# Optimization experiments

Measured on AMD Instinct MI355X. Metric: run time of the kernel, lower is better.

## Reference

```python
import jax, jax.numpy as jnp
import numpy as np

B, T, C = 8, 2048, 1024
E = 8            # num_experts (= world_size in the original)
K = 2            # top-k
CAP_FACTOR = 1.25
CAPACITY = int(T / E * CAP_FACTOR)  # 320, per (expert, batch-row)
DFF = 4 * C


def setup_inputs() -> dict:
    key = jax.random.key(0)
    ks = jax.random.split(key, 4)
    x = jax.random.normal(ks[0], (B, T, C), dtype=jnp.float32)
    Wg = jax.random.normal(ks[1], (C, E), dtype=jnp.float32) * (C ** -0.5)
    bg = jnp.zeros((E,), dtype=jnp.float32)
    W1 = jax.random.normal(ks[2], (E, C, DFF), dtype=jnp.float32) * (C ** -0.5)
    b1 = jnp.zeros((E, DFF), dtype=jnp.float32)
    W2 = jax.random.normal(ks[3], (E, DFF, C), dtype=jnp.float32) * (DFF ** -0.5)
    b2 = jnp.zeros((E, C), dtype=jnp.float32)
    return {"x": x, "Wg": Wg, "bg": bg, "W1": W1, "b1": b1, "W2": W2, "b2": b2}


def reference(x, Wg, bg, W1, b1, W2, b2):
    # Router: linear + softmax, then top-k gating
    probs = jax.nn.softmax(jnp.einsum('btc,ce->bte', x, Wg) + bg, axis=-1)  # [B,T,E]
    topk_p, topk_e = jax.lax.top_k(probs, K)                               # [B,T,K]

    S = T * K  # one "assignment" per (token, k-slot), row-major (t, k) order
    e_flat = topk_e.reshape(B, S)                      # expert id per assignment
    p_flat = topk_p.reshape(B, S)

    # Position of each assignment within its (batch-row, expert) group,
    # ordered by token position then k-slot (matches nonzero() row-major order).
    onehot = (e_flat[..., None] == jnp.arange(E)).astype(jnp.int32)        # [B,S,E]
    pos_all = jnp.cumsum(onehot, axis=1) - 1                                # [B,S,E]
    pos = jnp.take_along_axis(pos_all, e_flat[..., None], axis=2)[..., 0]   # [B,S]
    keep = pos < CAPACITY                               # overflow tokens are dropped

    # Dispatch tokens into padded per-(expert,row) buffers: [E,B,CAPACITY,C]
    x_rep = jnp.repeat(x, K, axis=1)                    # [B,S,C], assignment order
    b_idx = jnp.broadcast_to(jnp.arange(B)[:, None], (B, S))
    pos_scat = jnp.where(keep, pos, CAPACITY)           # out-of-range -> dropped
    dispatch = jnp.zeros((E, B, CAPACITY, C), dtype=x.dtype)
    dispatch = dispatch.at[e_flat, b_idx, pos_scat].set(x_rep, mode='drop')

    # Grouped expert FFN (padding rows are zeros; their outputs are never read back)
    h = jax.nn.relu(jnp.einsum('ebsc,ech->ebsh', dispatch, W1) + b1[:, None, None, :])
    y = jnp.einsum('ebsh,ehc->ebsc', h, W2) + b2[:, None, None, :]

    # Combine: gather back, scale by gate prob (dropped tokens -> padding_val 0)
    gathered = y[e_flat, b_idx, jnp.clip(pos, 0, CAPACITY - 1)]             # [B,S,C]
    out = gathered * jnp.where(keep, p_flat, 0.0)[..., None]
    return out.reshape(B, T, K, C).sum(axis=2)          # sum over k assignments
```

## Files before the change

### kernel.cpp

```cpp
#include <hip/hip_runtime.h>
#include <stdint.h>

#define B_ 8
#define T_ 2048
#define C_ 1024
#define E_ 8
#define K_ 2
#define CAP_ 320
#define DFF_ 4096
#define S_ (T_*K_)
#define NTOK (B_*T_)
#define ROWS_PER_E (B_*CAP_)

typedef __attribute__((ext_vector_type(8))) short short8;
typedef __attribute__((ext_vector_type(4))) float floatx4;

__device__ __forceinline__ unsigned short f2bf(float f) {
  union { float f; unsigned u; } v; v.f = f;
  unsigned r = v.u + 0x7fffu + ((v.u >> 16) & 1u);
  return (unsigned short)(r >> 16);
}
__device__ __forceinline__ float bf2f(unsigned short h) {
  union { unsigned u; float f; } v; v.u = ((unsigned)h) << 16;
  return v.f;
}

__global__ void router_kernel(const float* __restrict__ x, const float* __restrict__ Wg,
                              const float* __restrict__ bg,
                              int* __restrict__ topk_e, float* __restrict__ topk_p)
{
  int token = (int)((blockIdx.x * blockDim.x + threadIdx.x) >> 6);
  int lane = threadIdx.x & 63;
  if (token >= NTOK) return;
  const float* xr = x + (size_t)token * C_;
  double acc[E_];
  #pragma unroll
  for (int e = 0; e < E_; ++e) acc[e] = 0.0;
  for (int c = lane; c < C_; c += 64) {
    double xv = (double)xr[c];
    const float4* w4 = (const float4*)(Wg + (size_t)c * E_);
    float4 wa = w4[0], wb = w4[1];
    acc[0] += xv * (double)wa.x; acc[1] += xv * (double)wa.y;
    acc[2] += xv * (double)wa.z; acc[3] += xv * (double)wa.w;
    acc[4] += xv * (double)wb.x; acc[5] += xv * (double)wb.y;
    acc[6] += xv * (double)wb.z; acc[7] += xv * (double)wb.w;
  }
  #pragma unroll
  for (int off = 32; off; off >>= 1) {
    #pragma unroll
    for (int e = 0; e < E_; ++e) acc[e] += __shfl_down(acc[e], off, 64);
  }
  if (lane == 0) {
    double lg[E_];
    double mx = -1e300;
    #pragma unroll
    for (int e = 0; e < E_; ++e) { lg[e] = acc[e] + (double)bg[e]; mx = fmax(mx, lg[e]); }
    double se = 0.0, pr[E_];
    #pragma unroll
    for (int e = 0; e < E_; ++e) { pr[e] = exp(lg[e] - mx); se += pr[e]; }
    #pragma unroll
    for (int e = 0; e < E_; ++e) pr[e] /= se;
    int e0 = 0;
    #pragma unroll
    for (int e = 1; e < E_; ++e) if (pr[e] > pr[e0]) e0 = e;
    int e1 = -1;
    #pragma unroll
    for (int e = 0; e < E_; ++e) {
      if (e == e0) continue;
      if (e1 < 0 || pr[e] > pr[e1]) e1 = e;
    }
    topk_e[token*2+0] = e0; topk_p[token*2+0] = (float)pr[e0];
    topk_e[token*2+1] = e1; topk_p[token*2+1] = (float)pr[e1];
  }
}

__global__ void scan_kernel(const int* __restrict__ topk_e,
                            int* __restrict__ pos_arr,
                            int* __restrict__ slot_src,
                            int* __restrict__ counts)
{
  const int b = blockIdx.x;
  const int tid = threadIdx.x;
  const int PT = S_ / 256;
  __shared__ int cnt[256][E_];
  int e_loc[16];
  int local[E_];
  #pragma unroll
  for (int e = 0; e < E_; ++e) local[e] = 0;
  const int* te = topk_e + (size_t)b * S_;
  for (int j = 0; j < PT; ++j) {
    int e = te[tid*PT + j];
    e_loc[j] = e;
    local[e]++;
  }
  #pragma unroll
  for (int e = 0; e < E_; ++e) cnt[tid][e] = local[e];
  __syncthreads();
  if (tid < E_) {
    int run = 0;
    for (int i = 0; i < 256; ++i) { int v = cnt[i][tid]; cnt[i][tid] = run; run += v; }
    counts[tid*B_ + b] = run;
  }
  __syncthreads();
  int base[E_];
  #pragma unroll
  for (int e = 0; e < E_; ++e) base[e] = cnt[tid][e];
  for (int j = 0; j < PT; ++j) {
    int e = e_loc[j];
    int p = base[e]++;
    int s = tid*PT + j;
    if (p < CAP_) {
      pos_arr[(size_t)b*S_ + s] = p;
      slot_src[((size_t)e*B_ + b)*CAP_ + p] = s >> 1;
    } else {
      pos_arr[(size_t)b*S_ + s] = -1;
    }
  }
}

__global__ void transpose_conv_kernel(const float* __restrict__ in, unsigned short* __restrict__ out,
                                      int R, int Cc)
{
  __shared__ float tile[32][33];
  const int e = blockIdx.z;
  const float* ine = in + (size_t)e * R * Cc;
  unsigned short* oute = out + (size_t)e * R * Cc;
  const int c0 = blockIdx.x * 32, r0 = blockIdx.y * 32;
  const int tx = threadIdx.x & 7, ty = threadIdx.x >> 3;
  float4 v = *(const float4*)(ine + (size_t)(r0 + ty) * Cc + c0 + tx*4);
  tile[ty][tx*4+0] = v.x; tile[ty][tx*4+1] = v.y;
  tile[ty][tx*4+2] = v.z; tile[ty][tx*4+3] = v.w;
  __syncthreads();
  ushort4 o;
  o.x = f2bf(tile[tx*4+0][ty]);
  o.y = f2bf(tile[tx*4+1][ty]);
  o.z = f2bf(tile[tx*4+2][ty]);
  o.w = f2bf(tile[tx*4+3][ty]);
  *(ushort4*)(oute + (size_t)(c0 + ty) * R + r0 + tx*4) = o;
}

__global__ void dispatch_kernel(const float* __restrict__ x, const int* __restrict__ slot_src,
                                const int* __restrict__ counts, unsigned short* __restrict__ Xd,
                                int e_base, int nexp)
{
  int row = (int)((blockIdx.x * blockDim.x + threadIdx.x) >> 6);
  int lane = threadIdx.x & 63;
  int total = nexp * B_ * CAP_;
  if (row >= total) return;
  int el = row / (B_*CAP_);
  int rem = row - el*(B_*CAP_);
  int b = rem / CAP_, slot = rem - b*CAP_;
  int eg = e_base + el;
  int cnt = counts[eg*B_ + b]; if (cnt > CAP_) cnt = CAP_;
  unsigned short* orow = Xd + (size_t)row * C_;
  if (slot < cnt) {
    int t = slot_src[((size_t)eg*B_ + b)*CAP_ + slot];
    const float4* xr = (const float4*)(x + ((size_t)b*T_ + t)*C_);
    #pragma unroll
    for (int i = 0; i < C_/256; ++i) {
      float4 v = xr[i*64 + lane];
      ushort4 o;
      o.x = f2bf(v.x); o.y = f2bf(v.y); o.z = f2bf(v.z); o.w = f2bf(v.w);
      ((ushort4*)orow)[i*64 + lane] = o;
    }
  } else {
    ushort4 z; z.x = z.y = z.z = z.w = 0;
    #pragma unroll
    for (int i = 0; i < C_/256; ++i) ((ushort4*)orow)[i*64 + lane] = z;
  }
}

template<int RELU>
__global__ __launch_bounds__(256, 2) void gemm_bt_kernel(
    const unsigned short* __restrict__ A,
    const unsigned short* __restrict__ BT,
    const float* __restrict__ bias,
    unsigned short* __restrict__ Out,
    int M, int N, int K)
{
  __shared__ __align__(16) unsigned short ldsA[128*32];
  __shared__ __align__(16) unsigned short ldsB[128*32];
  const int e = blockIdx.z;
  const unsigned short* Ae = A + (size_t)e * M * K;
  const unsigned short* Be = BT + (size_t)e * N * K;
  const float* be = bias + (size_t)e * N;
  unsigned short* Oe = Out + (size_t)e * M * N;
  const int m0 = blockIdx.y * 128, n0 = blockIdx.x * 128;
  const int tid = threadIdx.x, lane = tid & 63, w = tid >> 6;
  const int wr = w >> 1, wc = w & 1;

  floatx4 acc[4][4];
  #pragma unroll
  for (int i = 0; i < 4; ++i)
    #pragma unroll
    for (int j = 0; j < 4; ++j) acc[i][j] = (floatx4){0.f, 0.f, 0.f, 0.f};

  const int c0 = tid, c1 = tid + 256;
  const int ar0 = c0 >> 2, ap0 = (c0 & 3) * 8;
  const int ar1 = c1 >> 2, ap1 = (c1 & 3) * 8;
  const unsigned short* agp0 = Ae + (size_t)(m0 + ar0)*K + ap0;
  const unsigned short* agp1 = Ae + (size_t)(m0 + ar1)*K + ap1;
  const unsigned short* bgp0 = Be + (size_t)(n0 + ar0)*K + ap0;
  const unsigned short* bgp1 = Be + (size_t)(n0 + ar1)*K + ap1;

  short8 sA0 = *(const short8*)(agp0);
  short8 sA1 = *(const short8*)(agp1);
  short8 sB0 = *(const short8*)(bgp0);
  short8 sB1 = *(const short8*)(bgp1);

  short8* wAp = (short8*)ldsA;
  short8* wBp = (short8*)ldsB;

  const int fRow = lane & 15, fK = (lane >> 4) * 8;
  const unsigned short* raBase = ldsA + (size_t)(wr*64 + fRow)*32 + fK;
  const unsigned short* rbBase = ldsB + (size_t)(wc*64 + fRow)*32 + fK;

  const int nk = K / 32;
  for (int kt = 0; kt < nk; ++kt) {
    __syncthreads();
    wAp[c0] = sA0; wAp[c1] = sA1;
    wBp[c0] = sB0; wBp[c1] = sB1;
    __syncthreads();
    if (kt + 1 < nk) {
      const int koff = (kt + 1) * 32;
      sA0 = *(const short8*)(agp0 + koff);
      sA1 = *(const short8*)(agp1 + koff);
      sB0 = *(const short8*)(bgp0 + koff);
      sB1 = *(const short8*)(bgp1 + koff);
    }
    short8 af[4], bf[4];
    #pragma unroll
    for (int m = 0; m < 4; ++m) af[m] = *(const short8*)(raBase + m*16*32);
    #pragma unroll
    for (int n = 0; n < 4; ++n) bf[n] = *(const short8*)(rbBase + n*16*32);
    #pragma unroll
    for (int m = 0; m < 4; ++m)
      #pragma unroll
      for (int n = 0; n < 4; ++n)
        acc[m][n] = __builtin_amdgcn_mfma_f32_16x16x32_bf16(af[m], bf[n], acc[m][n], 0, 0, 0);
  }

  const int col = lane & 15, rbase = (lane >> 4) * 4;
  #pragma unroll
  for (int m = 0; m < 4; ++m) {
    const int gr0 = m0 + wr*64 + m*16 + rbase;
    #pragma unroll
    for (int n = 0; n < 4; ++n) {
      const int gc = n0 + wc*64 + n*16 + col;
      const float bv = be[gc];
      #pragma unroll
      for (int r = 0; r < 4; ++r) {
        float v = acc[m][n][r] + bv;
        if (RELU) v = fmaxf(v, 0.f);
        Oe[(size_t)(gr0 + r)*N + gc] = f2bf(v);
      }
    }
  }
}

__global__ void combine_kernel(const unsigned short* __restrict__ Y,
                               const int* __restrict__ topk_e, const float* __restrict__ topk_p,
                               const int* __restrict__ pos_arr, float* __restrict__ out)
{
  int token = (int)((blockIdx.x * blockDim.x + threadIdx.x) >> 6);
  int lane = threadIdx.x & 63;
  if (token >= NTOK) return;
  int b = token / T_, t = token - b*T_;
  int s0 = b*S_ + t*2;
  float acc[16];
  #pragma unroll
  for (int i = 0; i < 16; ++i) acc[i] = 0.f;
  #pragma unroll
  for (int k = 0; k < 2; ++k) {
    int pos = pos_arr[s0 + k];
    if (pos < 0) continue;
    int e = topk_e[s0 + k];
    float p = topk_p[s0 + k];
    const unsigned short* yr = Y + (((size_t)e*B_ + b)*CAP_ + pos) * C_;
    #pragma unroll
    for (int i = 0; i < 4; ++i) {
      ushort4 v = ((const ushort4*)yr)[i*64 + lane];
      acc[i*4+0] += p * bf2f(v.x);
      acc[i*4+1] += p * bf2f(v.y);
      acc[i*4+2] += p * bf2f(v.z);
      acc[i*4+3] += p * bf2f(v.w);
    }
  }
  float4* orow = (float4*)(out + (size_t)token * C_);
  #pragma unroll
  for (int i = 0; i < 4; ++i) {
    float4 o;
    o.x = acc[i*4+0]; o.y = acc[i*4+1]; o.z = acc[i*4+2]; o.w = acc[i*4+3];
    orow[i*64 + lane] = o;
  }
}

extern "C" void kernel_launch(void* const* d_in, const int* in_sizes, int n_in,
                              void* d_out, int out_size, void* d_ws, size_t ws_size,
                              hipStream_t stream)
{
  const float* x  = (const float*)d_in[0];
  const float* Wg = (const float*)d_in[1];
  const float* bg = (const float*)d_in[2];
  const float* W1 = (const float*)d_in[3];
  const float* b1 = (const float*)d_in[4];
  const float* W2 = (const float*)d_in[5];
  const float* b2 = (const float*)d_in[6];
  float* out = (float*)d_out;

  char* ws = (char*)d_ws;
  size_t off = 0;
  auto alloc = [&](size_t bytes) -> char* {
    char* p = ws + off;
    off = (off + bytes + 255) & ~(size_t)255;
    return p;
  };
  int*   topk_e  = (int*)  alloc((size_t)NTOK * K_ * 4);
  float* topk_p  = (float*)alloc((size_t)NTOK * K_ * 4);
  int*   pos_arr = (int*)  alloc((size_t)B_ * S_ * 4);
  int*   slot_src= (int*)  alloc((size_t)E_ * B_ * CAP_ * 4);
  int*   counts  = (int*)  alloc((size_t)E_ * B_ * 4);
  unsigned short* Ybuf = (unsigned short*)alloc((size_t)E_ * ROWS_PER_E * C_ * 2);
  size_t fixed = off;
  const size_t perE = (size_t)C_ * DFF_ * 2
                    + (size_t)ROWS_PER_E * C_ * 2
                    + (size_t)ROWS_PER_E * DFF_ * 2
                    + 3 * 256;
  int k = 8;
  while (k > 1 && fixed + (size_t)k * perE > ws_size) k >>= 1;
  unsigned short* Wt = (unsigned short*)alloc((size_t)k * C_ * DFF_ * 2);
  unsigned short* Xd = (unsigned short*)alloc((size_t)k * ROWS_PER_E * C_ * 2);
  unsigned short* Hb = (unsigned short*)alloc((size_t)k * ROWS_PER_E * DFF_ * 2);

  router_kernel<<<NTOK/4, 256, 0, stream>>>(x, Wg, bg, topk_e, topk_p);
  scan_kernel<<<B_, 256, 0, stream>>>(topk_e, pos_arr, slot_src, counts);

  for (int eb = 0; eb < E_; eb += k) {
    transpose_conv_kernel<<<dim3(DFF_/32, C_/32, k), 256, 0, stream>>>(
        W1 + (size_t)eb * C_ * DFF_, Wt, C_, DFF_);
    dispatch_kernel<<<(k * ROWS_PER_E) / 4, 256, 0, stream>>>(x, slot_src, counts, Xd, eb, k);
    gemm_bt_kernel<1><<<dim3(DFF_/128, ROWS_PER_E/128, k), 256, 0, stream>>>(
        Xd, Wt, b1 + (size_t)eb * DFF_, Hb, ROWS_PER_E, DFF_, C_);
    transpose_conv_kernel<<<dim3(C_/32, DFF_/32, k), 256, 0, stream>>>(
        W2 + (size_t)eb * DFF_ * C_, Wt, DFF_, C_);
    gemm_bt_kernel<0><<<dim3(C_/128, ROWS_PER_E/128, k), 256, 0, stream>>>(
        Hb, Wt, b2 + (size_t)eb * C_, Ybuf + (size_t)eb * ROWS_PER_E * C_, ROWS_PER_E, C_, DFF_);
  }

  combine_kernel<<<NTOK/4, 256, 0, stream>>>(Ybuf, topk_e, topk_p, pos_arr, out);
}
```

Before: 652.1 us.

## Load GEMM tiles directly into LDS with global_load_lds and raise occupancy

The expert GEMM kernel no longer stages A/B tiles through registers. Each wave now issues 16-byte global_load_lds DMA writes straight into shared memory, placed after the fragments are read and before the MFMA loop so the next tile's fetch overlaps compute. Launch bounds go from 2 to 3 blocks per CU, since the staging registers are no longer needed. The schedule keeps a single LDS buffer, so it depends on the barriers correctly waiting for the async LDS writes to land.

```diff
diff --git a/kernel.cpp b/kernel.cpp
--- a/kernel.cpp
+++ b/kernel.cpp
@@ -24,6 +24,10 @@
   union { unsigned u; float f; } v; v.u = ((unsigned)h) << 16;
   return v.f;
 }
+
+#define GLOAD16(g, l) __builtin_amdgcn_global_load_lds( \
+    (const __attribute__((address_space(1))) void*)(g), \
+    (__attribute__((address_space(3))) void*)(l), 16, 0, 0)
 
 __global__ void router_kernel(const float* __restrict__ x, const float* __restrict__ Wg,
                               const float* __restrict__ bg,
@@ -171,7 +175,7 @@
 }
 
 template<int RELU>
-__global__ __launch_bounds__(256, 2) void gemm_bt_kernel(
+__global__ __launch_bounds__(256, 3) void gemm_bt_kernel(
     const unsigned short* __restrict__ A,
     const unsigned short* __restrict__ BT,
     const float* __restrict__ bias,
@@ -195,49 +199,50 @@
     #pragma unroll
     for (int j = 0; j < 4; ++j) acc[i][j] = (floatx4){0.f, 0.f, 0.f, 0.f};
 
-  const int c0 = tid, c1 = tid + 256;
-  const int ar0 = c0 >> 2, ap0 = (c0 & 3) * 8;
-  const int ar1 = c1 >> 2, ap1 = (c1 & 3) * 8;
-  const unsigned short* agp0 = Ae + (size_t)(m0 + ar0)*K + ap0;
-  const unsigned short* agp1 = Ae + (size_t)(m0 + ar1)*K + ap1;
-  const unsigned short* bgp0 = Be + (size_t)(n0 + ar0)*K + ap0;
-  const unsigned short* bgp1 = Be + (size_t)(n0 + ar1)*K + ap1;
-
-  short8 sA0 = *(const short8*)(agp0);
-  short8 sA1 = *(const short8*)(agp1);
-  short8 sB0 = *(const short8*)(bgp0);
-  short8 sB1 = *(const short8*)(bgp1);
-
-  short8* wAp = (short8*)ldsA;
-  short8* wBp = (short8*)ldsB;
+  const int cA0 = tid;
+  const int cA1 = 256 + tid;
+  const int r0c = cA0 >> 2, p0c = (cA0 & 3) * 8;
+  const int r1c = cA1 >> 2, p1c = (cA1 & 3) * 8;
+  const unsigned short* ga0 = Ae + (size_t)(m0 + r0c)*K + p0c;
+  const unsigned short* ga1 = Ae + (size_t)(m0 + r1c)*K + p1c;
+  const unsigned short* gb0 = Be + (size_t)(n0 + r0c)*K + p0c;
+  const unsigned short* gb1 = Be + (size_t)(n0 + r1c)*K + p1c;
+  unsigned short* laq0 = ldsA + (size_t)w * 512;
+  unsigned short* laq1 = ldsA + 2048 + (size_t)w * 512;
+  unsigned short* lbq0 = ldsB + (size_t)w * 512;
+  unsigned short* lbq1 = ldsB + 2048 + (size_t)w * 512;
 
   const int fRow = lane & 15, fK = (lane >> 4) * 8;
   const unsigned short* raBase = ldsA + (size_t)(wr*64 + fRow)*32 + fK;
   const unsigned short* rbBase = ldsB + (size_t)(wc*64 + fRow)*32 + fK;
 
   const int nk = K / 32;
+  GLOAD16(ga0, laq0);
+  GLOAD16(ga1, laq1);
+  GLOAD16(gb0, lbq0);
+  GLOAD16(gb1, lbq1);
+  __syncthreads();
+
   for (int kt = 0; kt < nk; ++kt) {
-    __syncthreads();
-    wAp[c0] = sA0; wAp[c1] = sA1;
-    wBp[c0] = sB0; wBp[c1] = sB1;
+    short8 af[4], bf[4];
+    #pragma unroll
+    for (int m = 0; m < 4; ++m) af[m] = *(const short8*)(raBase + m*512);
+    #pragma unroll
+    for (int n = 0; n < 4; ++n) bf[n] = *(const short8*)(rbBase + n*512);
     __syncthreads();
     if (kt + 1 < nk) {
       const int koff = (kt + 1) * 32;
-      sA0 = *(const short8*)(agp0 + koff);
-      sA1 = *(const short8*)(agp1 + koff);
-      sB0 = *(const short8*)(bgp0 + koff);
-      sB1 = *(const short8*)(bgp1 + koff);
-    }
-    short8 af[4], bf[4];
-    #pragma unroll
-    for (int m = 0; m < 4; ++m) af[m] = *(const short8*)(raBase + m*16*32);
-    #pragma unroll
-    for (int n = 0; n < 4; ++n) bf[n] = *(const short8*)(rbBase + n*16*32);
+      GLOAD16(ga0 + koff, laq0);
+      GLOAD16(ga1 + koff, laq1);
+      GLOAD16(gb0 + koff, lbq0);
+      GLOAD16(gb1 + koff, lbq1);
+    }
     #pragma unroll
     for (int m = 0; m < 4; ++m)
       #pragma unroll
       for (int n = 0; n < 4; ++n)
         acc[m][n] = __builtin_amdgcn_mfma_f32_16x16x32_bf16(af[m], bf[n], acc[m][n], 0, 0, 0);
+    __syncthreads();
   }
 
   const int col = lane & 15, rbase = (lane >> 4) * 4;
```

Result: no change. 645.2 us (-1.1%).
